# Performance work log

Measured on AMD Instinct MI355X. Metric: run time of the kernel, lower is better.

## Reference

```python
import jax, jax.numpy as jnp
import numpy as np

MAP_W = 500
EGO_H, EGO_W = 1024, 2048  # hardcoded interpolate target in memory_update


def resize_bilinear_align_corners(img, oh, ow):
    # img: [H, W, C] -> [oh, ow, C], matches torch bilinear align_corners=True
    h, w, _ = img.shape
    ys = jnp.linspace(0.0, h - 1.0, oh)
    xs = jnp.linspace(0.0, w - 1.0, ow)
    y0 = jnp.floor(ys).astype(jnp.int32)
    y1 = jnp.minimum(y0 + 1, h - 1)
    wy = (ys - y0.astype(ys.dtype))[:, None, None]
    x0 = jnp.floor(xs).astype(jnp.int32)
    x1 = jnp.minimum(x0 + 1, w - 1)
    wx = (xs - x0.astype(xs.dtype))[None, :, None]
    rows = img[y0] * (1.0 - wy) + img[y1] * wy          # [oh, W, C]
    out = rows[:, x0] * (1.0 - wx) + rows[:, x1] * wx    # [oh, ow, C]
    return out


def setup_inputs() -> dict:
    key = jax.random.key(0)
    k1, k2, k3, k4, k5 = jax.random.split(key, 5)
    features = jax.random.normal(k1, (1, 64, 128, 256), dtype=jnp.float32)
    proj_indices = jax.random.randint(k2, (250000,), 0, 500000, dtype=jnp.int64)
    masks_inliers = jax.random.bernoulli(k3, 0.5, (EGO_H, EGO_W))
    W_lin = jax.random.normal(k4, (256, 64), dtype=jnp.float32) * 0.05
    b_lin = jax.random.normal(k5, (256,), dtype=jnp.float32) * 0.01
    return {"features": features, "proj_indices": proj_indices,
            "masks_inliers": masks_inliers, "W_lin": W_lin, "b_lin": b_lin}


def reference(features, proj_indices, masks_inliers, W_lin, b_lin):
    # features: [1, C, h, w] egocentric encoder features
    # proj_indices: [MAP_W*MAP_W] indices into the compacted inlier pixels
    # masks_inliers: [EGO_H, EGO_W] bool
    C = features.shape[1]
    mem_dim = W_lin.shape[0]

    # torch: F.interpolate(feature, (1024, 2048), bilinear, align_corners=True)
    feat = jnp.transpose(features[0], (1, 2, 0))                 # [h, w, C]
    feat = resize_bilinear_align_corners(feat, EGO_H, EGO_W)     # [1024, 2048, C]
    feat_flat = feat.reshape(-1, C)                              # [HW, C]

    # torch: feature = feature[mask_inliers, :] compacts inlier pixels in
    # row-major order; proj_index addresses that compacted array. A stable
    # argsort of ~mask gives the pixel index of each compacted slot.
    mask_flat = masks_inliers.reshape(-1)
    positions = jnp.argsort(jnp.logical_not(mask_flat))          # inliers first, stable

    threshold = jnp.max(proj_indices)
    m = proj_indices < threshold                                  # [MAP_W*MAP_W]

    hw = EGO_H * EGO_W
    idx_pix = positions[jnp.clip(proj_indices, 0, hw - 1)]        # [MAP_W*MAP_W]
    gathered = feat_flat[idx_pix]                                 # [MAP_W*MAP_W, C]

    # mem_update == 'replace': state[m] = linlayer(gathered[m])
    mem = gathered @ W_lin.T + b_lin                              # [MAP_W*MAP_W, mem_dim]
    state = jnp.where(m[:, None], mem, jnp.zeros((), mem.dtype))

    memory = state.reshape(MAP_W, MAP_W, mem_dim)
    memory = jnp.transpose(memory, (2, 0, 1))[None]               # [1, mem_dim, 500, 500]
    observed_masks = m.reshape(1, MAP_W, MAP_W)
    return memory, observed_masks
```

## Files before the change

### kernel.cpp

```cpp
#include <hip/hip_runtime.h>
#include <hip/hip_bf16.h>

typedef unsigned short ushort_t;

#define MAPC 250000
#define NCH 2048
#define CHSZ 1024
#define NPOS 500000

#define OFF_SCAL   0
#define OFF_CNT    1024
#define OFF_POS    16384
#define OFF_FEATT  2016384
#define OFF_WF     6210688
#define OFF_BF     6276224

__device__ inline int mask_at(const void* m, int mode, int px) {
    if (mode == 0) return ((const unsigned char*)m)[px] != 0;
    if (mode == 2) return ((const ushort_t*)m)[px] != 0;
    return ((const int*)m)[px] != 0;
}

__device__ inline int proj_at(const int* p, int mode, int i) {
    return mode ? p[2 * i] : p[i];
}

__global__ void k_detect(const void* feats, const int* pj, const void* mbv,
                         const void* Wv, const void* bv,
                         float* __restrict__ Wf, float* __restrict__ bf,
                         int* __restrict__ scal) {
    __shared__ int s_insane, s_oddnz, s_non01, s_off4, s_low2;
    int t = threadIdx.x;
    if (t == 0) { s_insane = 0; s_oddnz = 0; s_non01 = 0; s_off4 = 0; s_low2 = 0; }
    __syncthreads();
    {
        ushort_t u = ((const ushort_t*)feats)[2 * t];
        int e = (u >> 7) & 0xFF;
        if (e < 0x66 || e > 0x8E) atomicAdd(&s_insane, 1);
    }
    if (t < 128) { if (pj[2 * t + 1] != 0) atomicAdd(&s_oddnz, 1); }
    for (int i = t; i < 512; i += 256) {
        unsigned char v = ((const unsigned char*)mbv)[i];
        if (v > 1) atomicAdd(&s_non01, 1);
        if ((i & 3) && v) atomicAdd(&s_off4, 1);
        if (((i & 3) < 2) && v) atomicAdd(&s_low2, 1);
    }
    __syncthreads();
    int f32m = (s_insane > 32) ? 1 : 0;
    if (t == 0) {
        scal[0] = -1;
        scal[2] = f32m;
        scal[3] = (s_oddnz == 0) ? 1 : 0;
        int mm;
        if (s_non01 == 0) mm = (s_off4 > 8) ? 0 : 1;
        else              mm = (s_low2 > 0) ? 2 : 1;
        scal[4] = mm;
    }
    if (f32m) {
        const float* W = (const float*)Wv; const float* b = (const float*)bv;
        for (int i = t; i < 256 * 64; i += 256) Wf[i] = W[i];
        bf[t] = b[t];
    } else {
        const __hip_bfloat16* W = (const __hip_bfloat16*)Wv;
        const __hip_bfloat16* b = (const __hip_bfloat16*)bv;
        for (int i = t; i < 256 * 64; i += 256) Wf[i] = __bfloat162float(W[i]);
        bf[t] = __bfloat162float(b[t]);
    }
}

__global__ void k_max(const int* __restrict__ proj, int* __restrict__ scal) {
    int mode = scal[3];
    int i = blockIdx.x * 256 + threadIdx.x;
    int v = (i < MAPC) ? proj_at(proj, mode, i) : -1;
    for (int o = 32; o; o >>= 1) v = max(v, __shfl_down(v, o, 64));
    if ((threadIdx.x & 63) == 0) atomicMax(scal, v);
}

__global__ void k_count(const void* __restrict__ mask, const int* __restrict__ scal,
                        int* __restrict__ cnt) {
    int mode = scal[4];
    int chunk = blockIdx.x, t = threadIdx.x;
    int c = 0;
    for (int i = 0; i < 4; ++i)
        c += mask_at(mask, mode, chunk * CHSZ + i * 256 + t);
    for (int o = 32; o; o >>= 1) c += __shfl_down(c, o, 64);
    __shared__ int ws4[4];
    if ((t & 63) == 0) ws4[t >> 6] = c;
    __syncthreads();
    if (t == 0) cnt[chunk] = ws4[0] + ws4[1] + ws4[2] + ws4[3];
}

__global__ void k_scan(int* __restrict__ cnt, int* __restrict__ scal) {
    __shared__ int part[256];
    int t = threadIdx.x;
    int base = t * 8;
    int loc[8];
    int s = 0;
    for (int i = 0; i < 8; ++i) { loc[i] = s; s += cnt[base + i]; }
    part[t] = s;
    __syncthreads();
    int mine = s;
    for (int off = 1; off < 256; off <<= 1) {
        int add = (t >= off) ? part[t - off] : 0;
        __syncthreads();
        part[t] += add;
        __syncthreads();
    }
    int incl = part[t];
    int excl = incl - mine;
    for (int i = 0; i < 8; ++i) cnt[base + i] = excl + loc[i];
    if (t == 255) scal[1] = incl;
}

__global__ void k_positions(const void* __restrict__ mask,
                            const int* __restrict__ cpre,
                            const int* __restrict__ scal,
                            int* __restrict__ positions) {
    int mode = scal[4];
    int chunk = blockIdx.x, t = threadIdx.x, w = t >> 6, lane = t & 63;
    int inBase = cpre[chunk];
    int outBase = chunk * CHSZ - inBase;
    int nin = scal[1];
    __shared__ int wsum[4];
    __shared__ int s_run;
    if (t == 0) s_run = 0;
    __syncthreads();
    for (int pass = 0; pass < 4; ++pass) {
        int q = pass * 256 + t;
        int px = chunk * CHSZ + q;
        bool isin = mask_at(mask, mode, px) != 0;
        unsigned long long bal = __ballot(isin);
        int before = __popcll(bal & ((1ULL << lane) - 1ULL));
        int wcnt = __popcll(bal);
        if (lane == 0) wsum[w] = wcnt;
        __syncthreads();
        int woff = 0;
        for (int ww = 0; ww < w; ++ww) woff += wsum[ww];
        int run = s_run;
        int in_rank = run + woff + before;
        int slot = isin ? (inBase + in_rank) : (nin + outBase + (q - in_rank));
        if (slot < NPOS) positions[slot] = px;
        __syncthreads();
        if (t == 0) s_run = run + wsum[0] + wsum[1] + wsum[2] + wsum[3];
        __syncthreads();
    }
}

__global__ void k_transpose(const void* __restrict__ feat,
                            const int* __restrict__ scal,
                            __hip_bfloat16* __restrict__ featT) {
    __shared__ ushort_t tile[64][65];
    int f32m = scal[2];
    int y = blockIdx.x >> 2;
    int xt = (blockIdx.x & 3) * 64;
    int t = threadIdx.x;
    ushort_t* fout = (ushort_t*)featT;
    int xl = t & 63, cq = t >> 6;
    if (f32m) {
        const float* fin = (const float*)feat;
        for (int i = 0; i < 16; ++i) {
            int c = cq * 16 + i;
            __hip_bfloat16 h = __float2bfloat16(fin[c * 32768 + y * 256 + xt + xl]);
            tile[c][xl] = *(ushort_t*)&h;
        }
    } else {
        const ushort_t* fin = (const ushort_t*)feat;
        for (int i = 0; i < 16; ++i) {
            int c = cq * 16 + i;
            tile[c][xl] = fin[c * 32768 + y * 256 + xt + xl];
        }
    }
    __syncthreads();
    int cl = t & 63, xq = t >> 6;
    for (int i = 0; i < 16; ++i) {
        int x = xq * 16 + i;
        fout[(y * 256 + xt + x) * 64 + cl] = tile[cl][x];
    }
}

__global__ __launch_bounds__(256) void k_main(
    const __hip_bfloat16* __restrict__ featT,
    const int* __restrict__ proj,
    const int* __restrict__ positions,
    const float* __restrict__ Wf,
    const float* __restrict__ bf,
    const int* __restrict__ scal,
    float* __restrict__ out_mem,
    float* __restrict__ out_obs)
{
    __shared__ float f_lds[64][65];
    __shared__ int s_pm[64];
    int t = threadIdx.x;
    int lane = t & 63;
    int w = t >> 6;
    int cellbase = blockIdx.x * 64;
    int thr = scal[0];
    int pmode = scal[3];

    if (t < 64) {
        int i = cellbase + t;
        int pm = -1;
        if (i < MAPC) {
            int pi = proj_at(proj, pmode, i);
            bool m = pi < thr;
            if (m) pm = positions[pi];
            out_obs[i] = m ? 1.0f : 0.0f;
        }
        s_pm[t] = pm;
    }
    __syncthreads();

    {
        int c = t & 63;
        int jq = t >> 6;
        for (int pass = 0; pass < 16; ++pass) {
            int j = pass * 4 + jq;
            int p = s_pm[j];
            float v = 0.0f;
            if (p >= 0) {
                int y = p >> 11, x = p & 2047;
                float fy = (float)y * (127.0f / 1023.0f);
                float fx = (float)x * (255.0f / 2047.0f);
                int y0 = (int)fy, x0 = (int)fx;
                float wy = fy - (float)y0, wx = fx - (float)x0;
                int y1 = min(y0 + 1, 127), x1 = min(x0 + 1, 255);
                const __hip_bfloat16* b00 = featT + (y0 * 256 + x0) * 64;
                const __hip_bfloat16* b01 = featT + (y0 * 256 + x1) * 64;
                const __hip_bfloat16* b10 = featT + (y1 * 256 + x0) * 64;
                const __hip_bfloat16* b11 = featT + (y1 * 256 + x1) * 64;
                float f00 = __bfloat162float(b00[c]);
                float f01 = __bfloat162float(b01[c]);
                float f10 = __bfloat162float(b10[c]);
                float f11 = __bfloat162float(b11[c]);
                float top = f00 + wx * (f01 - f00);
                float bot = f10 + wx * (f11 - f10);
                v = top + wy * (bot - top);
            }
            f_lds[j][c] = v;
        }
    }
    __syncthreads();

    float fr[64];
    #pragma unroll
    for (int cc = 0; cc < 64; ++cc) fr[cc] = f_lds[lane][cc];

    int pm_l = s_pm[lane];
    int cell = cellbase + lane;
    bool valid = cell < MAPC;
    int kbase = __builtin_amdgcn_readfirstlane(w) * 64;

    for (int kk = 0; kk < 64; kk += 2) {
        int k0 = kbase + kk;
        const float* w0 = Wf + k0 * 64;
        const float* w1 = w0 + 64;
        float a0 = 0.f, a1 = 0.f, a2 = 0.f, a3 = 0.f;
        #pragma unroll
        for (int cc = 0; cc < 64; cc += 2) {
            a0 += w0[cc]     * fr[cc];
            a1 += w0[cc + 1] * fr[cc + 1];
            a2 += w1[cc]     * fr[cc];
            a3 += w1[cc + 1] * fr[cc + 1];
        }
        float r0 = bf[k0] + a0 + a1;
        float r1 = bf[k0 + 1] + a2 + a3;
        if (pm_l < 0) { r0 = 0.f; r1 = 0.f; }
        if (valid) {
            out_mem[k0 * MAPC + cell]       = r0;
            out_mem[(k0 + 1) * MAPC + cell] = r1;
        }
    }
}

extern "C" void kernel_launch(void* const* d_in, const int* in_sizes, int n_in,
                              void* d_out, int out_size, void* d_ws, size_t ws_size,
                              hipStream_t stream) {
    const void* features = d_in[0];
    const int* proj = (const int*)d_in[1];
    const void* mask = d_in[2];
    const void* W = d_in[3];
    const void* b = d_in[4];

    char* ws = (char*)d_ws;
    int* scal = (int*)(ws + OFF_SCAL);
    int* cnt = (int*)(ws + OFF_CNT);
    int* positions = (int*)(ws + OFF_POS);
    __hip_bfloat16* featT = (__hip_bfloat16*)(ws + OFF_FEATT);
    float* Wf = (float*)(ws + OFF_WF);
    float* bf = (float*)(ws + OFF_BF);

    float* out_mem = (float*)d_out;
    float* out_obs = out_mem + 256 * MAPC;

    hipLaunchKernelGGL(k_detect, dim3(1), dim3(256), 0, stream,
                       features, proj, mask, W, b, Wf, bf, scal);
    hipLaunchKernelGGL(k_max, dim3((MAPC + 255) / 256), dim3(256), 0, stream, proj, scal);
    hipLaunchKernelGGL(k_count, dim3(NCH), dim3(256), 0, stream, mask, scal, cnt);
    hipLaunchKernelGGL(k_scan, dim3(1), dim3(256), 0, stream, cnt, scal);
    hipLaunchKernelGGL(k_positions, dim3(NCH), dim3(256), 0, stream, mask, cnt, scal, positions);
    hipLaunchKernelGGL(k_transpose, dim3(512), dim3(256), 0, stream, features, scal, featT);
    hipLaunchKernelGGL(k_main, dim3((MAPC + 63) / 64), dim3(256), 0, stream,
                       featT, proj, positions, Wf, bf, scal, out_mem, out_obs);
}
```

Baseline: 480.7 us.

## Compute linear layer with bf16 MFMA instead of scalar FP32 FMAs

Result: faster. 387.1 us (-19.5%).

```diff
diff --git a/kernel.cpp b/kernel.cpp
--- a/kernel.cpp
+++ b/kernel.cpp
@@ -2,6 +2,9 @@
 #include <hip/hip_bf16.h>
 
 typedef unsigned short ushort_t;
+typedef unsigned int uint_t;
+typedef __attribute__((ext_vector_type(8))) short short8;
+typedef __attribute__((ext_vector_type(4))) float floatx4;
 
 #define MAPC 250000
 #define NCH 2048
@@ -12,8 +15,8 @@
 #define OFF_CNT    1024
 #define OFF_POS    16384
 #define OFF_FEATT  2016384
-#define OFF_WF     6210688
-#define OFF_BF     6276224
+#define OFF_WH     6210688
+#define OFF_BF     6243456
 
 __device__ inline int mask_at(const void* m, int mode, int px) {
     if (mode == 0) return ((const unsigned char*)m)[px] != 0;
@@ -27,7 +30,7 @@
 
 __global__ void k_detect(const void* feats, const int* pj, const void* mbv,
                          const void* Wv, const void* bv,
-                         float* __restrict__ Wf, float* __restrict__ bf,
+                         ushort_t* __restrict__ Wh, float* __restrict__ bfl,
                          int* __restrict__ scal) {
     __shared__ int s_insane, s_oddnz, s_non01, s_off4, s_low2;
     int t = threadIdx.x;
@@ -58,13 +61,16 @@
     }
     if (f32m) {
         const float* W = (const float*)Wv; const float* b = (const float*)bv;
-        for (int i = t; i < 256 * 64; i += 256) Wf[i] = W[i];
-        bf[t] = b[t];
+        for (int i = t; i < 256 * 64; i += 256) {
+            __hip_bfloat16 h = __float2bfloat16(W[i]);
+            Wh[i] = *(ushort_t*)&h;
+        }
+        bfl[t] = b[t];
     } else {
-        const __hip_bfloat16* W = (const __hip_bfloat16*)Wv;
+        const ushort_t* W = (const ushort_t*)Wv;
         const __hip_bfloat16* b = (const __hip_bfloat16*)bv;
-        for (int i = t; i < 256 * 64; i += 256) Wf[i] = __bfloat162float(W[i]);
-        bf[t] = __bfloat162float(b[t]);
+        for (int i = t; i < 256 * 64; i += 256) Wh[i] = W[i];
+        bfl[t] = __bfloat162float(b[t]);
     }
 }
 
@@ -182,20 +188,24 @@
     const __hip_bfloat16* __restrict__ featT,
     const int* __restrict__ proj,
     const int* __restrict__ positions,
-    const float* __restrict__ Wf,
-    const float* __restrict__ bf,
+    const ushort_t* __restrict__ Wh,
+    const float* __restrict__ bfl,
     const int* __restrict__ scal,
     float* __restrict__ out_mem,
     float* __restrict__ out_obs)
 {
-    __shared__ float f_lds[64][65];
+    __shared__ ushort_t B_lds[64 * 72];
     __shared__ int s_pm[64];
+    __shared__ float s_bias[256];
     int t = threadIdx.x;
-    int lane = t & 63;
+    int r15 = t & 15;
+    int quad = (t >> 4) & 3;
     int w = t >> 6;
     int cellbase = blockIdx.x * 64;
     int thr = scal[0];
     int pmode = scal[3];
+
+    s_bias[t] = bfl[t];
 
     if (t < 64) {
         int i = cellbase + t;
@@ -211,12 +221,12 @@
     __syncthreads();
 
     {
-        int c = t & 63;
-        int jq = t >> 6;
-        for (int pass = 0; pass < 16; ++pass) {
-            int j = pass * 4 + jq;
+        int cp = t & 31;
+        int jq = t >> 5;
+        for (int pass = 0; pass < 8; ++pass) {
+            int j = pass * 8 + jq;
             int p = s_pm[j];
-            float v = 0.0f;
+            float v0 = 0.0f, v1 = 0.0f;
             if (p >= 0) {
                 int y = p >> 11, x = p & 2047;
                 float fy = (float)y * (127.0f / 1023.0f);
@@ -224,50 +234,69 @@
                 int y0 = (int)fy, x0 = (int)fx;
                 float wy = fy - (float)y0, wx = fx - (float)x0;
                 int y1 = min(y0 + 1, 127), x1 = min(x0 + 1, 255);
-                const __hip_bfloat16* b00 = featT + (y0 * 256 + x0) * 64;
-                const __hip_bfloat16* b01 = featT + (y0 * 256 + x1) * 64;
-                const __hip_bfloat16* b10 = featT + (y1 * 256 + x0) * 64;
-                const __hip_bfloat16* b11 = featT + (y1 * 256 + x1) * 64;
-                float f00 = __bfloat162float(b00[c]);
-                float f01 = __bfloat162float(b01[c]);
-                float f10 = __bfloat162float(b10[c]);
-                float f11 = __bfloat162float(b11[c]);
-                float top = f00 + wx * (f01 - f00);
-                float bot = f10 + wx * (f11 - f10);
-                v = top + wy * (bot - top);
+                const uint_t* p00 = (const uint_t*)(featT + (y0 * 256 + x0) * 64);
+                const uint_t* p01 = (const uint_t*)(featT + (y0 * 256 + x1) * 64);
+                const uint_t* p10 = (const uint_t*)(featT + (y1 * 256 + x0) * 64);
+                const uint_t* p11 = (const uint_t*)(featT + (y1 * 256 + x1) * 64);
+                uint_t u00 = p00[cp], u01 = p01[cp], u10 = p10[cp], u11 = p11[cp];
+                float f00l = __uint_as_float(u00 << 16), f00h = __uint_as_float(u00 & 0xFFFF0000u);
+                float f01l = __uint_as_float(u01 << 16), f01h = __uint_as_float(u01 & 0xFFFF0000u);
+                float f10l = __uint_as_float(u10 << 16), f10h = __uint_as_float(u10 & 0xFFFF0000u);
+                float f11l = __uint_as_float(u11 << 16), f11h = __uint_as_float(u11 & 0xFFFF0000u);
+                float topl = f00l + wx * (f01l - f00l);
+                float botl = f10l + wx * (f11l - f10l);
+                v0 = topl + wy * (botl - topl);
+                float toph = f00h + wx * (f01h - f00h);
+                float both = f10h + wx * (f11h - f10h);
+                v1 = toph + wy * (both - toph);
             }
-            f_lds[j][c] = v;
-        }
-    }
-    __syncthreads();
-
-    float fr[64];
+            __hip_bfloat16 h0 = __float2bfloat16(v0);
+            __hip_bfloat16 h1 = __float2bfloat16(v1);
+            uint_t packed = ((uint_t)(*(ushort_t*)&h1) << 16) | (uint_t)(*(ushort_t*)&h0);
+            *(uint_t*)&B_lds[j * 72 + cp * 2] = packed;
+        }
+    }
+    __syncthreads();
+
+    int chb = __builtin_amdgcn_readfirstlane(w) * 64;
+    short8 afr[4][2];
     #pragma unroll
-    for (int cc = 0; cc < 64; ++cc) fr[cc] = f_lds[lane][cc];
-
-    int pm_l = s_pm[lane];
-    int cell = cellbase + lane;
-    bool valid = cell < MAPC;
-    int kbase = __builtin_amdgcn_readfirstlane(w) * 64;
-
-    for (int kk = 0; kk < 64; kk += 2) {
-        int k0 = kbase + kk;
-        const float* w0 = Wf + k0 * 64;
-        const float* w1 = w0 + 64;
-        float a0 = 0.f, a1 = 0.f, a2 = 0.f, a3 = 0.f;
+    for (int mt = 0; mt < 4; ++mt)
         #pragma unroll
-        for (int cc = 0; cc < 64; cc += 2) {
-            a0 += w0[cc]     * fr[cc];
-            a1 += w0[cc + 1] * fr[cc + 1];
-            a2 += w1[cc]     * fr[cc];
-            a3 += w1[cc + 1] * fr[cc + 1];
-        }
-        float r0 = bf[k0] + a0 + a1;
-        float r1 = bf[k0 + 1] + a2 + a3;
-        if (pm_l < 0) { r0 = 0.f; r1 = 0.f; }
-        if (valid) {
-            out_mem[k0 * MAPC + cell]       = r0;
-            out_mem[(k0 + 1) * MAPC + cell] = r1;
+        for (int ks = 0; ks < 2; ++ks)
+            afr[mt][ks] = *(const short8*)(Wh + (chb + mt * 16 + r15) * 64 + ks * 32 + quad * 8);
+
+    floatx4 acc[4][4];
+    #pragma unroll
+    for (int mt = 0; mt < 4; ++mt)
+        #pragma unroll
+        for (int nt = 0; nt < 4; ++nt)
+            acc[mt][nt] = (floatx4){0.f, 0.f, 0.f, 0.f};
+
+    #pragma unroll
+    for (int nt = 0; nt < 4; ++nt) {
+        short8 b0 = *(const short8*)&B_lds[(nt * 16 + r15) * 72 + quad * 8];
+        short8 b1 = *(const short8*)&B_lds[(nt * 16 + r15) * 72 + 32 + quad * 8];
+        #pragma unroll
+        for (int mt = 0; mt < 4; ++mt) {
+            acc[mt][nt] = __builtin_amdgcn_mfma_f32_16x16x32_bf16(afr[mt][0], b0, acc[mt][nt], 0, 0, 0);
+            acc[mt][nt] = __builtin_amdgcn_mfma_f32_16x16x32_bf16(afr[mt][1], b1, acc[mt][nt], 0, 0, 0);
+        }
+    }
+
+    #pragma unroll
+    for (int nt = 0; nt < 4; ++nt) {
+        int cell = cellbase + nt * 16 + r15;
+        bool ok = cell < MAPC;
+        float z = (s_pm[nt * 16 + r15] < 0) ? 0.0f : 1.0f;
+        #pragma unroll
+        for (int mt = 0; mt < 4; ++mt) {
+            int ch0 = chb + mt * 16 + quad * 4;
+            #pragma unroll
+            for (int reg = 0; reg < 4; ++reg) {
+                float r = (acc[mt][nt][reg] + s_bias[ch0 + reg]) * z;
+                if (ok) out_mem[(size_t)(ch0 + reg) * MAPC + cell] = r;
+            }
         }
     }
 }
@@ -286,19 +315,19 @@
     int* cnt = (int*)(ws + OFF_CNT);
     int* positions = (int*)(ws + OFF_POS);
     __hip_bfloat16* featT = (__hip_bfloat16*)(ws + OFF_FEATT);
-    float* Wf = (float*)(ws + OFF_WF);
-    float* bf = (float*)(ws + OFF_BF);
+    ushort_t* Wh = (ushort_t*)(ws + OFF_WH);
+    float* bfl = (float*)(ws + OFF_BF);
 
     float* out_mem = (float*)d_out;
-    float* out_obs = out_mem + 256 * MAPC;
+    float* out_obs = out_mem + (size_t)256 * MAPC;
 
     hipLaunchKernelGGL(k_detect, dim3(1), dim3(256), 0, stream,
-                       features, proj, mask, W, b, Wf, bf, scal);
+                       features, proj, mask, W, b, Wh, bfl, scal);
     hipLaunchKernelGGL(k_max, dim3((MAPC + 255) / 256), dim3(256), 0, stream, proj, scal);
     hipLaunchKernelGGL(k_count, dim3(NCH), dim3(256), 0, stream, mask, scal, cnt);
     hipLaunchKernelGGL(k_scan, dim3(1), dim3(256), 0, stream, cnt, scal);
     hipLaunchKernelGGL(k_positions, dim3(NCH), dim3(256), 0, stream, mask, cnt, scal, positions);
     hipLaunchKernelGGL(k_transpose, dim3(512), dim3(256), 0, stream, features, scal, featT);
     hipLaunchKernelGGL(k_main, dim3((MAPC + 63) / 64), dim3(256), 0, stream,
-                       featT, proj, positions, Wf, bf, scal, out_mem, out_obs);
-}
+                       featT, proj, positions, Wh, bfl, scal, out_mem, out_obs);
+}
```
